# Performance work log

Measured on AMD Instinct MI355X. Metric: run time of the kernel, lower is better.

## Reference

```python
import jax, jax.numpy as jnp
import numpy as np

B, N, D = 8, 1024, 1024
H = 16
HD = D // H  # 64
SCALE = float(HD) ** -0.5


def setup_inputs() -> dict:
    key = jax.random.key(0)
    k1, k2, k3 = jax.random.split(key, 3)
    x = jax.random.normal(k1, (B, N, D), dtype=jnp.float32)
    W_qkv = jax.random.normal(k2, (D, 3 * D), dtype=jnp.float32) * (D ** -0.5)
    b_qkv = jnp.zeros((3 * D,), dtype=jnp.float32)
    W_o = jax.random.normal(k3, (D, D), dtype=jnp.float32) * (D ** -0.5)
    b_o = jnp.zeros((D,), dtype=jnp.float32)
    return {"x": x, "W_qkv": W_qkv, "b_qkv": b_qkv, "W_o": W_o, "b_o": b_o}


def reference(x, W_qkv, b_qkv, W_o, b_o):
    b, n, _ = x.shape
    qkv = x @ W_qkv + b_qkv                      # (B, N, 3D)
    qkv = qkv.reshape(b, n, H, 3 * HD).transpose(0, 2, 1, 3)  # (B, H, N, 3*HD)
    q, k, v = jnp.split(qkv, 3, axis=-1)          # each (B, H, N, HD)
    attn = jnp.einsum('bhnd,bhmd->bhnm', q, k) * SCALE
    attn = jax.nn.softmax(attn, axis=-1)          # (B, H, N, N); dropout p=0 -> identity
    heads = jnp.einsum('bhnm,bhmd->bhnd', attn, v)
    heads = heads.transpose(0, 2, 1, 3).reshape(b, n, H * HD)  # (B, N, D)
    return heads @ W_o + b_o
```

## Files before the change

kernel.cpp:

```cpp
#include <hip/hip_runtime.h>
#include <hip/hip_bf16.h>

typedef unsigned short ushort_t;
typedef __bf16 bf16x8 __attribute__((ext_vector_type(8)));
typedef float floatx4 __attribute__((ext_vector_type(4)));

#define MFMA(a, b, c) __builtin_amdgcn_mfma_f32_16x16x32_bf16(a, b, c, 0, 0, 0)

__device__ __forceinline__ float b2f(ushort_t u) {
    union { ushort_t u; __hip_bfloat16 h; } cvt; cvt.u = u; return __bfloat162float(cvt.h);
}
__device__ __forceinline__ ushort_t f2b(float f) {
    union { ushort_t u; __hip_bfloat16 h; } cvt; cvt.h = __float2bfloat16(f); return cvt.u;
}

__device__ __forceinline__ void async_copy16(const ushort_t* g, ushort_t* l) {
    __builtin_amdgcn_global_load_lds(
        (const __attribute__((address_space(1))) void*)g,
        (__attribute__((address_space(3))) void*)l, 16, 0, 0);
}

__global__ void prep(const float* __restrict__ xin, ushort_t* __restrict__ xb,
                     const float* __restrict__ Wqkv, ushort_t* __restrict__ WqkvT,
                     const float* __restrict__ Wo, ushort_t* __restrict__ WoT) {
    __shared__ float tile[32][33];
    int bb = blockIdx.x;
    if (bb < 4096) {
        int i = bb * 256 + threadIdx.x;
        const float4* xf = (const float4*)xin;
        float4 a = xf[i * 2], b = xf[i * 2 + 1];
        union { ushort_t s[8]; uint4 v; } p;
        p.s[0] = f2b(a.x); p.s[1] = f2b(a.y); p.s[2] = f2b(a.z); p.s[3] = f2b(a.w);
        p.s[4] = f2b(b.x); p.s[5] = f2b(b.y); p.s[6] = f2b(b.z); p.s[7] = f2b(b.w);
        ((uint4*)xb)[i] = p.v;
    } else if (bb < 7168) {
        int b2 = bb - 4096;
        int p0 = (b2 % 96) * 32, k0 = (b2 / 96) * 32;
        int which = p0 >> 10, rem = p0 & 1023;
        int n0 = (rem >> 6) * 192 + which * 64 + (rem & 63);
        int tx = threadIdx.x & 31, ty = threadIdx.x >> 5;
#pragma unroll
        for (int i = 0; i < 4; ++i)
            tile[ty + i * 8][tx] = Wqkv[(size_t)(k0 + ty + i * 8) * 3072 + n0 + tx];
        __syncthreads();
#pragma unroll
        for (int i = 0; i < 4; ++i)
            WqkvT[(size_t)(p0 + ty + i * 8) * 1024 + k0 + tx] = f2b(tile[tx][ty + i * 8]);
    } else {
        int b3 = bb - 7168;
        int n0 = (b3 & 31) * 32, k0 = (b3 >> 5) * 32;
        int tx = threadIdx.x & 31, ty = threadIdx.x >> 5;
#pragma unroll
        for (int i = 0; i < 4; ++i)
            tile[ty + i * 8][tx] = Wo[(size_t)(k0 + ty + i * 8) * 1024 + n0 + tx];
        __syncthreads();
#pragma unroll
        for (int i = 0; i < 4; ++i)
            WoT[(size_t)(n0 + ty + i * 8) * 1024 + k0 + tx] = f2b(tile[tx][ty + i * 8]);
    }
}

__device__ __forceinline__ int tswz(int n, int m) {
    return n * 128 + (((m >> 3) ^ (n & 15)) << 3) + (m & 7);
}

__global__ __launch_bounds__(256, 4) void gemm_qkv(
    const ushort_t* __restrict__ A,
    const ushort_t* __restrict__ Bt,
    const float* __restrict__ bias,
    ushort_t* __restrict__ Qb, ushort_t* __restrict__ Kb, ushort_t* __restrict__ Vtb) {
    const int K = 1024;
    __shared__ __align__(16) ushort_t SH[16384];
    ushort_t* Alds = SH;
    ushort_t* Blds = SH + 8192;
    int tid = threadIdx.x;
    int wave = tid >> 6, lane = tid & 63;
    int quad = lane >> 4, l16 = lane & 15;
    int wm = (wave >> 1) * 64, wn = (wave & 1) * 64;
    int m0 = blockIdx.x * 128, n0 = blockIdx.y * 128;

    floatx4 acc[4][4] = {};

    int srow[4], scol[4];
#pragma unroll
    for (int p = 0; p < 4; ++p) {
        int slot = (wave * 4 + p) * 64 + lane;
        int row = slot >> 3;
        srow[p] = row;
        scol[p] = ((slot & 7) ^ (row & 7)) * 8;
    }

    for (int kt = 0; kt < 16; ++kt) {
        int k0 = kt * 64;
        __syncthreads();
#pragma unroll
        for (int p = 0; p < 4; ++p) {
            int t = wave * 4 + p;
            async_copy16(&A[(m0 + srow[p]) * K + k0 + scol[p]], &Alds[t * 512]);
            async_copy16(&Bt[(n0 + srow[p]) * K + k0 + scol[p]], &Blds[t * 512]);
        }
        __syncthreads();
#pragma unroll
        for (int ki = 0; ki < 2; ++ki) {
            bf16x8 af[4], bfv[4];
            int sc = ((ki * 4 + quad) ^ (l16 & 7)) * 8;
#pragma unroll
            for (int i = 0; i < 4; ++i) {
                __builtin_memcpy(&af[i],  &Alds[(wm + i * 16 + l16) * 64 + sc], 16);
                __builtin_memcpy(&bfv[i], &Blds[(wn + i * 16 + l16) * 64 + sc], 16);
            }
#pragma unroll
            for (int i = 0; i < 4; ++i)
#pragma unroll
                for (int j = 0; j < 4; ++j)
                    acc[i][j] = MFMA(af[i], bfv[j], acc[i][j]);
        }
    }

    int which = n0 >> 10;
    int b = m0 >> 10;

    if (which < 2) {
        ushort_t* dst = which ? Kb : Qb;
        float sc = which ? 1.0f : 0.18033688f;
#pragma unroll
        for (int j = 0; j < 4; ++j) {
            int C = n0 + wn + j * 16 + l16;
            int c = C & 1023;
            int h = c >> 6, d = c & 63;
            float bv = bias[((C >> 6) & 15) * 192 + which * 64 + (C & 63)];
            size_t hb = (size_t)(b * 16 + h) * 65536 + d;
#pragma unroll
            for (int i = 0; i < 4; ++i)
#pragma unroll
                for (int g = 0; g < 4; ++g) {
                    int n_tok = (m0 & 1023) + wm + i * 16 + quad * 4 + g;
                    dst[hb + (size_t)n_tok * 64] = f2b((acc[i][j][g] + bv) * sc);
                }
        }
    } else {
        __syncthreads();
#pragma unroll
        for (int j = 0; j < 4; ++j) {
            int C = n0 + wn + j * 16 + l16;
            int nl2 = wn + j * 16 + l16;
            float bv = bias[((C >> 6) & 15) * 192 + 128 + (C & 63)];
#pragma unroll
            for (int i = 0; i < 4; ++i)
#pragma unroll
                for (int g = 0; g < 4; ++g) {
                    int ml = wm + i * 16 + quad * 4 + g;
                    SH[tswz(nl2, ml)] = f2b(acc[i][j][g] + bv);
                }
        }
        __syncthreads();
        int r = tid >> 1, half = tid & 1;
        int vcol = (n0 - 2048) + r;
        int h = vcol >> 6, d = vcol & 63;
        size_t base = ((size_t)(b * 16 + h) * 64 + d) * 1024 + (m0 & 1023) + half * 64;
#pragma unroll
        for (int i8 = 0; i8 < 8; ++i8) {
            int chunk = half * 8 + i8;
            uint4 v;
            __builtin_memcpy(&v, &SH[r * 128 + ((chunk ^ (r & 15)) << 3)], 16);
            __builtin_memcpy(&Vtb[base + i8 * 8], &v, 16);
        }
    }
}

__global__ __launch_bounds__(256, 4) void attn(
    const ushort_t* __restrict__ Qb, const ushort_t* __restrict__ Kb,
    const ushort_t* __restrict__ Vtb, ushort_t* __restrict__ heads) {
    __shared__ __align__(16) ushort_t Klds[4096];
    __shared__ __align__(16) ushort_t Vlds[4096];
    __shared__ __align__(16) ushort_t Plds[128 * 76];
    int tid = threadIdx.x;
    int wave = tid >> 6, lane = tid & 63;
    int quad = lane >> 4, l16 = lane & 15;

    int slot = blockIdx.y + 16 * blockIdx.z;
    int bh = blockIdx.x + 8 * (slot >> 3);
    int qx = slot & 7;
    int b = bh >> 4, h = bh & 15;
    const ushort_t* Qh = Qb + (size_t)bh * 65536;
    const ushort_t* Kh = Kb + (size_t)bh * 65536;
    const ushort_t* Vh = Vtb + (size_t)bh * 65536;

    bf16x8 qa[2][2];
#pragma unroll
    for (int mi = 0; mi < 2; ++mi) {
        int qrow = qx * 128 + wave * 32 + mi * 16 + l16;
        __builtin_memcpy(&qa[mi][0], &Qh[qrow * 64 + quad * 8], 16);
        __builtin_memcpy(&qa[mi][1], &Qh[qrow * 64 + 32 + quad * 8], 16);
    }

    floatx4 oacc[2][4] = {};
    floatx4 oext[2] = {};

    bf16x8 onesfrag;
    {
        ushort_t v = (l16 == 0) ? (ushort_t)0x3F80 : (ushort_t)0;
        ushort_t tmp[8] = {v, v, v, v, v, v, v, v};
        __builtin_memcpy(&onesfrag, tmp, 16);
    }

    int srow[2], scol[2];
#pragma unroll
    for (int p = 0; p < 2; ++p) {
        int slot2 = (wave * 2 + p) * 64 + lane;
        int row = slot2 >> 3;
        srow[p] = row;
        scol[p] = ((slot2 & 7) ^ (row & 7)) * 8;
    }

    for (int kt = 0; kt < 16; ++kt) {
        int k0 = kt * 64;
        __syncthreads();
#pragma unroll
        for (int p = 0; p < 2; ++p) {
            int t = wave * 2 + p;
            async_copy16(&Kh[(k0 + srow[p]) * 64 + scol[p]], &Klds[t * 512]);
            async_copy16(&Vh[srow[p] * 1024 + k0 + scol[p]], &Vlds[t * 512]);
        }
        __syncthreads();

        bf16x8 kf[4][2];
#pragma unroll
        for (int n = 0; n < 4; ++n)
#pragma unroll
            for (int ki = 0; ki < 2; ++ki) {
                int sc = ((ki * 4 + quad) ^ (l16 & 7)) * 8;
                __builtin_memcpy(&kf[n][ki], &Klds[(n * 16 + l16) * 64 + sc], 16);
            }
#pragma unroll
        for (int mi = 0; mi < 2; ++mi)
#pragma unroll
            for (int n = 0; n < 4; ++n) {
                floatx4 z = {0.f, 0.f, 0.f, 0.f};
#pragma unroll
                for (int ki = 0; ki < 2; ++ki)
                    z = MFMA(kf[n][ki], qa[mi][ki], z);
                union { ushort_t s[4]; double d8; } pk;
#pragma unroll
                for (int g = 0; g < 4; ++g)
                    pk.s[g] = f2b(__builtin_exp2f(z[g]));
                __builtin_memcpy(
                    &Plds[(wave * 32 + mi * 16 + l16) * 76 + n * 16 + quad * 4],
                    &pk, 8);
            }

        bf16x8 vf[4][2];
#pragma unroll
        for (int n = 0; n < 4; ++n)
#pragma unroll
            for (int ki = 0; ki < 2; ++ki) {
                int sc = ((ki * 4 + quad) ^ (l16 & 7)) * 8;
                __builtin_memcpy(&vf[n][ki], &Vlds[(n * 16 + l16) * 64 + sc], 16);
            }
#pragma unroll
        for (int mi = 0; mi < 2; ++mi) {
            bf16x8 pa[2];
            int prow = wave * 32 + mi * 16 + l16;
#pragma unroll
            for (int ki = 0; ki < 2; ++ki)
                __builtin_memcpy(&pa[ki], &Plds[prow * 76 + ki * 32 + quad * 8], 16);
            __builtin_amdgcn_s_setprio(1);
#pragma unroll
            for (int n = 0; n < 4; ++n)
#pragma unroll
                for (int ki = 0; ki < 2; ++ki)
                    oacc[mi][n] = MFMA(pa[ki], vf[n][ki], oacc[mi][n]);
#pragma unroll
            for (int ki = 0; ki < 2; ++ki)
                oext[mi] = MFMA(pa[ki], onesfrag, oext[mi]);
            __builtin_amdgcn_s_setprio(0);
        }
    }

#pragma unroll
    for (int mi = 0; mi < 2; ++mi)
#pragma unroll
        for (int g = 0; g < 4; ++g) {
            float l = __shfl(oext[mi][g], (lane & 48));
            float inv = 1.f / l;
            int n_tok = qx * 128 + wave * 32 + mi * 16 + quad * 4 + g;
#pragma unroll
            for (int n = 0; n < 4; ++n)
                heads[(size_t)(b * 1024 + n_tok) * 1024 + h * 64 + n * 16 + l16] =
                    f2b(oacc[mi][n][g] * inv);
        }
}

__global__ __launch_bounds__(256, 4) void gemm_out(
    const ushort_t* __restrict__ A,
    const ushort_t* __restrict__ Bt,
    const float* __restrict__ bias,
    float* __restrict__ out) {
    const int K = 1024;
    __shared__ __align__(16) ushort_t Alds[128 * 64];
    __shared__ __align__(16) ushort_t Blds[128 * 64];
    int tid = threadIdx.x;
    int wave = tid >> 6, lane = tid & 63;
    int quad = lane >> 4, l16 = lane & 15;
    int wm = (wave >> 1) * 64, wn = (wave & 1) * 64;
    int m0 = blockIdx.x * 128, n0 = blockIdx.y * 128;

    floatx4 acc[4][4] = {};

    int srow[4], scol[4];
#pragma unroll
    for (int p = 0; p < 4; ++p) {
        int slot = (wave * 4 + p) * 64 + lane;
        int row = slot >> 3;
        srow[p] = row;
        scol[p] = ((slot & 7) ^ (row & 7)) * 8;
    }

    for (int kt = 0; kt < 16; ++kt) {
        int k0 = kt * 64;
        __syncthreads();
#pragma unroll
        for (int p = 0; p < 4; ++p) {
            int t = wave * 4 + p;
            async_copy16(&A[(m0 + srow[p]) * K + k0 + scol[p]], &Alds[t * 512]);
            async_copy16(&Bt[(n0 + srow[p]) * K + k0 + scol[p]], &Blds[t * 512]);
        }
        __syncthreads();
#pragma unroll
        for (int ki = 0; ki < 2; ++ki) {
            bf16x8 af[4], bfv[4];
            int sc = ((ki * 4 + quad) ^ (l16 & 7)) * 8;
#pragma unroll
            for (int i = 0; i < 4; ++i) {
                __builtin_memcpy(&af[i],  &Alds[(wm + i * 16 + l16) * 64 + sc], 16);
                __builtin_memcpy(&bfv[i], &Blds[(wn + i * 16 + l16) * 64 + sc], 16);
            }
#pragma unroll
            for (int i = 0; i < 4; ++i)
#pragma unroll
                for (int j = 0; j < 4; ++j)
                    acc[i][j] = MFMA(af[i], bfv[j], acc[i][j]);
        }
    }

#pragma unroll
    for (int j = 0; j < 4; ++j) {
        int C = n0 + wn + j * 16 + l16;
        float bv = bias[C];
#pragma unroll
        for (int i = 0; i < 4; ++i)
#pragma unroll
            for (int g = 0; g < 4; ++g) {
                int R = m0 + wm + i * 16 + quad * 4 + g;
                out[(size_t)R * 1024 + C] = acc[i][j][g] + bv;
            }
    }
}

extern "C" void kernel_launch(void* const* d_in, const int* in_sizes, int n_in,
                              void* d_out, int out_size, void* d_ws, size_t ws_size,
                              hipStream_t stream) {
    const float* x    = (const float*)d_in[0];
    const float* Wqkv = (const float*)d_in[1];
    const float* bqkv = (const float*)d_in[2];
    const float* Wo   = (const float*)d_in[3];
    const float* bo   = (const float*)d_in[4];

    char* ws = (char*)d_ws;
    const size_t MB = 1u << 20;
    ushort_t* xb    = (ushort_t*)(ws);
    ushort_t* Qb    = (ushort_t*)(ws + 16 * MB);
    ushort_t* Kb    = (ushort_t*)(ws + 32 * MB);
    ushort_t* Vtb   = (ushort_t*)(ws + 48 * MB);
    ushort_t* WqkvT = (ushort_t*)(ws + 64 * MB);
    ushort_t* WoT   = (ushort_t*)(ws + 70 * MB);
    ushort_t* heads = (ushort_t*)(ws);

    prep<<<8192, 256, 0, stream>>>(x, xb, Wqkv, WqkvT, Wo, WoT);
    gemm_qkv<<<dim3(64, 24), 256, 0, stream>>>(xb, WqkvT, bqkv, Qb, Kb, Vtb);
    attn<<<dim3(8, 16, 8), 256, 0, stream>>>(Qb, Kb, Vtb, heads);
    gemm_out<<<dim3(64, 8), 256, 0, stream>>>(heads, WoT, bo, (float*)d_out);
}
```

Baseline: 232.9 us.

## Double-buffer K/V tiles and reuse the consumed K buffer for P

```diff
diff --git a/kernel.cpp b/kernel.cpp
--- a/kernel.cpp
+++ b/kernel.cpp
@@ -7,11 +7,8 @@
 
 #define MFMA(a, b, c) __builtin_amdgcn_mfma_f32_16x16x32_bf16(a, b, c, 0, 0, 0)
 
-__device__ __forceinline__ float b2f(ushort_t u) {
-    union { ushort_t u; __hip_bfloat16 h; } cvt; cvt.u = u; return __bfloat162float(cvt.h);
-}
 __device__ __forceinline__ ushort_t f2b(float f) {
-    union { ushort_t u; __hip_bfloat16 h; } cvt; cvt.h = __float2bfloat16(f); return cvt.u;
+    union { ushort_t u; __bf16 h; } cvt; cvt.h = (__bf16)f; return cvt.u;
 }
 
 __device__ __forceinline__ void async_copy16(const ushort_t* g, ushort_t* l) {
@@ -171,9 +168,7 @@
 __global__ __launch_bounds__(256, 4) void attn(
     const ushort_t* __restrict__ Qb, const ushort_t* __restrict__ Kb,
     const ushort_t* __restrict__ Vtb, ushort_t* __restrict__ heads) {
-    __shared__ __align__(16) ushort_t Klds[4096];
-    __shared__ __align__(16) ushort_t Vlds[4096];
-    __shared__ __align__(16) ushort_t Plds[128 * 76];
+    __shared__ __align__(16) ushort_t KV[2][2][4096];
     int tid = threadIdx.x;
     int wave = tid >> 6, lane = tid & 63;
     int quad = lane >> 4, l16 = lane & 15;
@@ -213,16 +208,23 @@
         scol[p] = ((slot2 & 7) ^ (row & 7)) * 8;
     }
 
+#pragma unroll
+    for (int p = 0; p < 2; ++p) {
+        int t = wave * 2 + p;
+        async_copy16(&Kh[srow[p] * 64 + scol[p]], &KV[0][0][t * 512]);
+        async_copy16(&Vh[srow[p] * 1024 + scol[p]], &KV[0][1][t * 512]);
+    }
+
+    int prot = l16 * 4;
+    int prow64 = (wave * 16 + l16) * 64;
+
     for (int kt = 0; kt < 16; ++kt) {
-        int k0 = kt * 64;
-        __syncthreads();
-#pragma unroll
-        for (int p = 0; p < 2; ++p) {
-            int t = wave * 2 + p;
-            async_copy16(&Kh[(k0 + srow[p]) * 64 + scol[p]], &Klds[t * 512]);
-            async_copy16(&Vh[srow[p] * 1024 + k0 + scol[p]], &Vlds[t * 512]);
-        }
-        __syncthreads();
+        int cur = kt & 1;
+
+        asm volatile("s_waitcnt vmcnt(0)" ::: "memory");
+        __builtin_amdgcn_sched_barrier(0);
+        __builtin_amdgcn_s_barrier();
+        __builtin_amdgcn_sched_barrier(0);
 
         bf16x8 kf[4][2];
 #pragma unroll
@@ -230,10 +232,36 @@
 #pragma unroll
             for (int ki = 0; ki < 2; ++ki) {
                 int sc = ((ki * 4 + quad) ^ (l16 & 7)) * 8;
-                __builtin_memcpy(&kf[n][ki], &Klds[(n * 16 + l16) * 64 + sc], 16);
-            }
-#pragma unroll
-        for (int mi = 0; mi < 2; ++mi)
+                __builtin_memcpy(&kf[n][ki], &KV[cur][0][(n * 16 + l16) * 64 + sc], 16);
+            }
+
+        if (kt < 15) {
+            int nk0 = (kt + 1) * 64, nb = cur ^ 1;
+#pragma unroll
+            for (int p = 0; p < 2; ++p) {
+                int t = wave * 2 + p;
+                async_copy16(&Kh[(nk0 + srow[p]) * 64 + scol[p]], &KV[nb][0][t * 512]);
+                async_copy16(&Vh[srow[p] * 1024 + nk0 + scol[p]], &KV[nb][1][t * 512]);
+            }
+        }
+
+        asm volatile("s_waitcnt lgkmcnt(0)" ::: "memory");
+        __builtin_amdgcn_sched_barrier(0);
+        __builtin_amdgcn_s_barrier();
+        __builtin_amdgcn_sched_barrier(0);
+
+        bf16x8 vf[4][2];
+#pragma unroll
+        for (int n = 0; n < 4; ++n)
+#pragma unroll
+            for (int ki = 0; ki < 2; ++ki) {
+                int sc = ((ki * 4 + quad) ^ (l16 & 7)) * 8;
+                __builtin_memcpy(&vf[n][ki], &KV[cur][1][(n * 16 + l16) * 64 + sc], 16);
+            }
+
+        ushort_t* Pl = &KV[cur][0][0];
+#pragma unroll
+        for (int mi = 0; mi < 2; ++mi) {
 #pragma unroll
             for (int n = 0; n < 4; ++n) {
                 floatx4 z = {0.f, 0.f, 0.f, 0.f};
@@ -244,26 +272,18 @@
 #pragma unroll
                 for (int g = 0; g < 4; ++g)
                     pk.s[g] = f2b(__builtin_exp2f(z[g]));
-                __builtin_memcpy(
-                    &Plds[(wave * 32 + mi * 16 + l16) * 76 + n * 16 + quad * 4],
-                    &pk, 8);
-            }
-
-        bf16x8 vf[4][2];
-#pragma unroll
-        for (int n = 0; n < 4; ++n)
+                __builtin_memcpy(&Pl[prow64 + ((n * 16 + quad * 4 + prot) & 63)],
+                                 &pk, 8);
+            }
+            bf16x8 pa[2];
 #pragma unroll
             for (int ki = 0; ki < 2; ++ki) {
-                int sc = ((ki * 4 + quad) ^ (l16 & 7)) * 8;
-                __builtin_memcpy(&vf[n][ki], &Vlds[(n * 16 + l16) * 64 + sc], 16);
-            }
-#pragma unroll
-        for (int mi = 0; mi < 2; ++mi) {
-            bf16x8 pa[2];
-            int prow = wave * 32 + mi * 16 + l16;
-#pragma unroll
-            for (int ki = 0; ki < 2; ++ki)
-                __builtin_memcpy(&pa[ki], &Plds[prow * 76 + ki * 32 + quad * 8], 16);
+                double lo, hi;
+                __builtin_memcpy(&lo, &Pl[prow64 + ((ki * 32 + quad * 8 + prot) & 63)], 8);
+                __builtin_memcpy(&hi, &Pl[prow64 + ((ki * 32 + quad * 8 + 4 + prot) & 63)], 8);
+                double t2[2] = {lo, hi};
+                __builtin_memcpy(&pa[ki], t2, 16);
+            }
             __builtin_amdgcn_s_setprio(1);
 #pragma unroll
             for (int n = 0; n < 4; ++n)
```

After: 330.7 us. +42.0%, slower.
